# Performance work log

Hardware: AMD Instinct MI355X
Metric: run time of the kernel (lower is better)

Reference implementation:

```python
import jax, jax.numpy as jnp
import numpy as np

B, C, L, D = 32, 1, 1024, 128


def _attention_matrix(x0, x1):
    # x0, x1: [B, 1, L, D]. A[b,0,i,j] = 1 / (1 + ||x0[b,0,i] - x1[b,0,j]||_2)
    a = x0[:, 0]  # [B, L, D]
    b = x1[:, 0]  # [B, L, D]
    # cdist via expansion: ||a_i - b_j||^2 = |a_i|^2 + |b_j|^2 - 2 a_i . b_j
    sq_a = jnp.sum(a * a, axis=-1)                      # [B, L]
    sq_b = jnp.sum(b * b, axis=-1)                      # [B, L]
    inner = jnp.einsum('bid,bjd->bij', a, b)            # [B, L, L]
    d2 = jnp.maximum(sq_a[:, :, None] + sq_b[:, None, :] - 2.0 * inner, 0.0)
    dist = jnp.sqrt(d2)
    A = 1.0 / (1.0 + dist)                              # [B, L, L]
    return A[:, None, :, :]                             # [B, 1, L, L]


def setup_inputs() -> dict:
    key = jax.random.key(0)
    k0, k1, kw0, kw1 = jax.random.split(key, 4)
    x0 = jax.random.normal(k0, (B, C, L, D), dtype=jnp.float32)
    x1 = jax.random.normal(k1, (B, C, L, D), dtype=jnp.float32)
    W0 = jax.random.normal(kw0, (L, D), dtype=jnp.float32)
    W1 = jax.random.normal(kw1, (L, D), dtype=jnp.float32)
    return {"x0": x0, "x1": x1, "W0": W0, "W1": W1}


def reference(x0, x1, W0, W1):
    A = _attention_matrix(x0, x1)                 # [B, 1, L, L]
    A_t = jnp.swapaxes(A, -1, -2)                 # [B, 1, L, L]
    a0 = jnp.matmul(A, W0)                        # [B, 1, L, D]
    a1 = jnp.matmul(A_t, W1)                      # [B, 1, L, D]
    f0 = jnp.concatenate([x0, a0], axis=1)        # [B, 2, L, D]
    f1 = jnp.concatenate([x1, a1], axis=1)        # [B, 2, L, D]
    return (f0, f1)
```

## Files before the change

### kernel.cpp

```cpp
#include <hip/hip_runtime.h>

#define B_ 32
#define L_ 1024
#define D_ 128
#define NT 256

typedef __attribute__((ext_vector_type(8))) short bf8_t;
typedef __attribute__((ext_vector_type(4))) short bf4_t;
typedef __attribute__((ext_vector_type(4))) float f4_t;

__device__ __forceinline__ unsigned cvtpk(float lo, float hi) {
  unsigned r;
  asm("v_cvt_pk_bf16_f32 %0, %1, %2" : "=v"(r) : "v"(lo), "v"(hi));
  return r;
}

__device__ __forceinline__ void gload16(const void* g, void* l) {
  __builtin_amdgcn_global_load_lds((const __attribute__((address_space(1))) void*)g,
                                   (__attribute__((address_space(3))) void*)l, 16, 0, 0);
}

__global__ __launch_bounds__(256)
void prep_kernel(const float* __restrict__ x0, const float* __restrict__ x1,
                 const float* __restrict__ W0, const float* __restrict__ W1,
                 short* __restrict__ Xs, float* __restrict__ sq,
                 short* __restrict__ Wt, float* __restrict__ out) {
  int bid = blockIdx.x;
  if (bid < 8192) {
    int t = bid * 256 + threadIdx.x;
    int row_id = t >> 5;
    int qp = t & 31;
    int which = row_id >> 15;
    int b = (row_id >> 10) & 31;
    int row = row_id & 1023;
    const float* x = which ? x1 : x0;
    float4 v = *(const float4*)(x + ((size_t)b * L_ + row) * D_ + qp * 4);
    float* o = out + (size_t)which * (B_ * 2 * L_ * D_) + (size_t)b * (2 * L_ * D_)
             + (size_t)row * D_ + qp * 4;
    *(float4*)o = v;
    unsigned w0 = cvtpk(v.x, v.y), w1 = cvtpk(v.z, v.w);
    char* xb = (char*)Xs + (size_t)row_id * 256 + ((qp * 8) ^ ((row & 7) << 4));
    *(uint2*)xb = make_uint2(w0, w1);
    float s = v.x * v.x + v.y * v.y + v.z * v.z + v.w * v.w;
    s += __shfl_xor(s, 1); s += __shfl_xor(s, 2); s += __shfl_xor(s, 4);
    s += __shfl_xor(s, 8); s += __shfl_xor(s, 16);
    if (qp == 0) sq[row_id] = s;
  } else {
    int idx = (bid - 8192) * 256 + threadIdx.x;
    int which = idx >> 17;
    int rm = idx & 131071;
    int j32 = rm >> 12;
    int d = (rm >> 5) & 127;
    int jj = rm & 31;
    const float* W = which ? W1 : W0;
    float wv = W[(j32 * 32 + jj) * D_ + d];
    Wt[idx] = (short)(cvtpk(wv, wv) & 0xffffu);
  }
}

__global__ __launch_bounds__(NT, 4)
void fused_attnconv(const short* __restrict__ Xs, const float* __restrict__ sq,
                    const short* __restrict__ Wt, float* __restrict__ out) {
  __shared__ char smem[28672];
  char* Pb = smem + 16384;
  float* sqyL = (float*)(smem + 24576);

  const int bid = blockIdx.x;
  const int x = bid & 7, g = bid >> 3;
  const int p = x + 8 * (g >> 4);
  const int it = g & 15;
  const int which = p >> 5, b = p & 31;
  const int i0 = it * 64;
  const int po = (which ^ 1) * 32 + b;

  const char* apanel = (const char*)Xs + (size_t)p * (L_ * 256);
  const char* ypanel = (const char*)Xs + (size_t)po * (L_ * 256);
  const float* sqx_p = sq + p * L_;
  const float* sqy_p = sq + po * L_;
  float* Oc1 = out + (size_t)which * (B_ * 2 * L_ * D_) + (size_t)b * (2 * L_ * D_) + (L_ * D_);

  const int tid = threadIdx.x;
  const int lane = tid & 63;
  const int w = tid >> 6;
  const int l15 = lane & 15;
  const int q = lane >> 4;
  const int I0 = w * 16;
  const int swz = (l15 & 7) << 4;

  const int yo0 = l15 * 256 + ((0 * 64 + q * 16) ^ swz);
  const int yo1 = l15 * 256 + ((1 * 64 + q * 16) ^ swz);
  const int yo2 = l15 * 256 + ((2 * 64 + q * 16) ^ swz);
  const int yo3 = l15 * 256 + ((3 * 64 + q * 16) ^ swz);
  const int pw0 = (I0 + l15) * 128 + ((q * 8) ^ swz);
  const int pw1 = (I0 + l15) * 128 + ((32 + q * 8) ^ swz);
  const int pro = (I0 + l15) * 128 + ((q * 16) ^ swz);

  bf8_t afr[4];
#pragma unroll
  for (int kb = 0; kb < 4; ++kb)
    afr[kb] = *(const bf8_t*)(apanel + (size_t)(i0 + I0 + l15) * 256 + ((kb * 64 + q * 16) ^ swz));
  const float sxv = sqx_p[i0 + I0 + l15];

  const short* wptr = Wt + which * 131072 + l15 * 32 + q * 8;
  const char* ypref = ypanel + 8192 + (size_t)tid * 16;
  const float* syp = sqyL + q * 4;

  *(f4_t*)(sqyL + tid * 4) = *(const f4_t*)(sqy_p + tid * 4);
  gload16(ypanel + (size_t)tid * 16, smem + tid * 16);
  gload16(ypanel + 4096 + (size_t)tid * 16, smem + 4096 + tid * 16);

  f4_t z4 = {0.f, 0.f, 0.f, 0.f};
  f4_t acc[8];
#pragma unroll
  for (int m = 0; m < 8; ++m) acc[m] = z4;

  __syncthreads();

#pragma unroll 1
  for (int jt = 0; jt < 32; ++jt) {
    char* yB = smem + (jt & 1) * 8192;

    bf8_t wf[8];
#pragma unroll
    for (int m = 0; m < 8; ++m)
      wf[m] = *(const bf8_t*)(wptr + m * 512);
    wptr += 4096;

    if (jt < 31) {
      char* yN = smem + ((jt + 1) & 1) * 8192;
      gload16(ypref, yN + tid * 16);
      gload16(ypref + 4096, yN + 4096 + tid * 16);
    }
    ypref += 8192;

    f4_t sy0 = *(const f4_t*)(syp);
    f4_t sy1 = *(const f4_t*)(syp + 16);
    syp += 32;

    f4_t ST0 = z4, ST1 = z4;
    {
      bf8_t ya = *(const bf8_t*)(yB + yo0);
      bf8_t yb = *(const bf8_t*)(yB + 4096 + yo0);
      ST0 = __builtin_amdgcn_mfma_f32_16x16x32_bf16(ya, afr[0], ST0, 0, 0, 0);
      ST1 = __builtin_amdgcn_mfma_f32_16x16x32_bf16(yb, afr[0], ST1, 0, 0, 0);
      ya = *(const bf8_t*)(yB + yo1);
      yb = *(const bf8_t*)(yB + 4096 + yo1);
      ST0 = __builtin_amdgcn_mfma_f32_16x16x32_bf16(ya, afr[1], ST0, 0, 0, 0);
      ST1 = __builtin_amdgcn_mfma_f32_16x16x32_bf16(yb, afr[1], ST1, 0, 0, 0);
      ya = *(const bf8_t*)(yB + yo2);
      yb = *(const bf8_t*)(yB + 4096 + yo2);
      ST0 = __builtin_amdgcn_mfma_f32_16x16x32_bf16(ya, afr[2], ST0, 0, 0, 0);
      ST1 = __builtin_amdgcn_mfma_f32_16x16x32_bf16(yb, afr[2], ST1, 0, 0, 0);
      ya = *(const bf8_t*)(yB + yo3);
      yb = *(const bf8_t*)(yB + 4096 + yo3);
      ST0 = __builtin_amdgcn_mfma_f32_16x16x32_bf16(ya, afr[3], ST0, 0, 0, 0);
      ST1 = __builtin_amdgcn_mfma_f32_16x16x32_bf16(yb, afr[3], ST1, 0, 0, 0);
    }

    {
      float A0 = __builtin_amdgcn_rcpf(1.0f + __builtin_amdgcn_sqrtf(fmaxf(__builtin_fmaf(-2.f, ST0[0], sxv + sy0[0]), 0.f)));
      float A1 = __builtin_amdgcn_rcpf(1.0f + __builtin_amdgcn_sqrtf(fmaxf(__builtin_fmaf(-2.f, ST0[1], sxv + sy0[1]), 0.f)));
      float A2 = __builtin_amdgcn_rcpf(1.0f + __builtin_amdgcn_sqrtf(fmaxf(__builtin_fmaf(-2.f, ST0[2], sxv + sy0[2]), 0.f)));
      float A3 = __builtin_amdgcn_rcpf(1.0f + __builtin_amdgcn_sqrtf(fmaxf(__builtin_fmaf(-2.f, ST0[3], sxv + sy0[3]), 0.f)));
      union { uint2 u; bf4_t s; } p0;
      p0.u = make_uint2(cvtpk(A0, A1), cvtpk(A2, A3));
      *(bf4_t*)(Pb + pw0) = p0.s;
      float B0 = __builtin_amdgcn_rcpf(1.0f + __builtin_amdgcn_sqrtf(fmaxf(__builtin_fmaf(-2.f, ST1[0], sxv + sy1[0]), 0.f)));
      float B1 = __builtin_amdgcn_rcpf(1.0f + __builtin_amdgcn_sqrtf(fmaxf(__builtin_fmaf(-2.f, ST1[1], sxv + sy1[1]), 0.f)));
      float B2 = __builtin_amdgcn_rcpf(1.0f + __builtin_amdgcn_sqrtf(fmaxf(__builtin_fmaf(-2.f, ST1[2], sxv + sy1[2]), 0.f)));
      float B3 = __builtin_amdgcn_rcpf(1.0f + __builtin_amdgcn_sqrtf(fmaxf(__builtin_fmaf(-2.f, ST1[3], sxv + sy1[3]), 0.f)));
      union { uint2 u; bf4_t s; } p1;
      p1.u = make_uint2(cvtpk(B0, B1), cvtpk(B2, B3));
      *(bf4_t*)(Pb + pw1) = p1.s;
    }

    asm volatile("" ::: "memory");
    __builtin_amdgcn_sched_barrier(0);

    {
      bf8_t pf = *(const bf8_t*)(Pb + pro);
#pragma unroll
      for (int m = 0; m < 8; ++m)
        acc[m] = __builtin_amdgcn_mfma_f32_16x16x32_bf16(pf, wf[m], acc[m], 0, 0, 0);
    }

    __syncthreads();
  }

#pragma unroll
  for (int m = 0; m < 8; ++m) {
    const int d = m * 16 + l15;
#pragma unroll
    for (int r = 0; r < 4; ++r)
      Oc1[(size_t)(i0 + I0 + q * 4 + r) * D_ + d] = acc[m][r];
  }
}

extern "C" void kernel_launch(void* const* d_in, const int* in_sizes, int n_in,
                              void* d_out, int out_size, void* d_ws, size_t ws_size,
                              hipStream_t stream) {
  const float* x0 = (const float*)d_in[0];
  const float* x1 = (const float*)d_in[1];
  const float* W0 = (const float*)d_in[2];
  const float* W1 = (const float*)d_in[3];
  float* out = (float*)d_out;

  char* ws = (char*)d_ws;
  short* Wt = (short*)ws;
  short* Xs = (short*)(ws + 524288);
  float* sq = (float*)(ws + 524288 + 16777216);

  prep_kernel<<<9216, 256, 0, stream>>>(x0, x1, W0, W1, Xs, sq, Wt, out);
  fused_attnconv<<<1024, NT, 0, stream>>>(Xs, sq, Wt, out);
}
```

Measured before the change: 90.46 us.

## Read Y tiles directly from global memory instead of LDS double buffer

```diff
diff --git a/kernel.cpp b/kernel.cpp
--- a/kernel.cpp
+++ b/kernel.cpp
@@ -13,11 +13,6 @@
   unsigned r;
   asm("v_cvt_pk_bf16_f32 %0, %1, %2" : "=v"(r) : "v"(lo), "v"(hi));
   return r;
-}
-
-__device__ __forceinline__ void gload16(const void* g, void* l) {
-  __builtin_amdgcn_global_load_lds((const __attribute__((address_space(1))) void*)g,
-                                   (__attribute__((address_space(3))) void*)l, 16, 0, 0);
 }
 
 __global__ __launch_bounds__(256)
@@ -61,9 +56,7 @@
 __global__ __launch_bounds__(NT, 4)
 void fused_attnconv(const short* __restrict__ Xs, const float* __restrict__ sq,
                     const short* __restrict__ Wt, float* __restrict__ out) {
-  __shared__ char smem[28672];
-  char* Pb = smem + 16384;
-  float* sqyL = (float*)(smem + 24576);
+  __shared__ char Pb[8192];
 
   const int bid = blockIdx.x;
   const int x = bid & 7, g = bid >> 3;
@@ -102,36 +95,21 @@
   const float sxv = sqx_p[i0 + I0 + l15];
 
   const short* wptr = Wt + which * 131072 + l15 * 32 + q * 8;
-  const char* ypref = ypanel + 8192 + (size_t)tid * 16;
-  const float* syp = sqyL + q * 4;
-
-  *(f4_t*)(sqyL + tid * 4) = *(const f4_t*)(sqy_p + tid * 4);
-  gload16(ypanel + (size_t)tid * 16, smem + tid * 16);
-  gload16(ypanel + 4096 + (size_t)tid * 16, smem + 4096 + tid * 16);
+  const char* ytile = ypanel;
+  const float* syp = sqy_p + q * 4;
 
   f4_t z4 = {0.f, 0.f, 0.f, 0.f};
   f4_t acc[8];
 #pragma unroll
   for (int m = 0; m < 8; ++m) acc[m] = z4;
 
-  __syncthreads();
-
 #pragma unroll 1
   for (int jt = 0; jt < 32; ++jt) {
-    char* yB = smem + (jt & 1) * 8192;
-
     bf8_t wf[8];
 #pragma unroll
     for (int m = 0; m < 8; ++m)
       wf[m] = *(const bf8_t*)(wptr + m * 512);
     wptr += 4096;
-
-    if (jt < 31) {
-      char* yN = smem + ((jt + 1) & 1) * 8192;
-      gload16(ypref, yN + tid * 16);
-      gload16(ypref + 4096, yN + 4096 + tid * 16);
-    }
-    ypref += 8192;
 
     f4_t sy0 = *(const f4_t*)(syp);
     f4_t sy1 = *(const f4_t*)(syp + 16);
@@ -139,23 +117,24 @@
 
     f4_t ST0 = z4, ST1 = z4;
     {
-      bf8_t ya = *(const bf8_t*)(yB + yo0);
-      bf8_t yb = *(const bf8_t*)(yB + 4096 + yo0);
+      bf8_t ya = *(const bf8_t*)(ytile + yo0);
+      bf8_t yb = *(const bf8_t*)(ytile + 4096 + yo0);
       ST0 = __builtin_amdgcn_mfma_f32_16x16x32_bf16(ya, afr[0], ST0, 0, 0, 0);
       ST1 = __builtin_amdgcn_mfma_f32_16x16x32_bf16(yb, afr[0], ST1, 0, 0, 0);
-      ya = *(const bf8_t*)(yB + yo1);
-      yb = *(const bf8_t*)(yB + 4096 + yo1);
+      ya = *(const bf8_t*)(ytile + yo1);
+      yb = *(const bf8_t*)(ytile + 4096 + yo1);
       ST0 = __builtin_amdgcn_mfma_f32_16x16x32_bf16(ya, afr[1], ST0, 0, 0, 0);
       ST1 = __builtin_amdgcn_mfma_f32_16x16x32_bf16(yb, afr[1], ST1, 0, 0, 0);
-      ya = *(const bf8_t*)(yB + yo2);
-      yb = *(const bf8_t*)(yB + 4096 + yo2);
+      ya = *(const bf8_t*)(ytile + yo2);
+      yb = *(const bf8_t*)(ytile + 4096 + yo2);
       ST0 = __builtin_amdgcn_mfma_f32_16x16x32_bf16(ya, afr[2], ST0, 0, 0, 0);
       ST1 = __builtin_amdgcn_mfma_f32_16x16x32_bf16(yb, afr[2], ST1, 0, 0, 0);
-      ya = *(const bf8_t*)(yB + yo3);
-      yb = *(const bf8_t*)(yB + 4096 + yo3);
+      ya = *(const bf8_t*)(ytile + yo3);
+      yb = *(const bf8_t*)(ytile + 4096 + yo3);
       ST0 = __builtin_amdgcn_mfma_f32_16x16x32_bf16(ya, afr[3], ST0, 0, 0, 0);
       ST1 = __builtin_amdgcn_mfma_f32_16x16x32_bf16(yb, afr[3], ST1, 0, 0, 0);
     }
+    ytile += 8192;
 
     {
       float A0 = __builtin_amdgcn_rcpf(1.0f + __builtin_amdgcn_sqrtf(fmaxf(__builtin_fmaf(-2.f, ST0[0], sxv + sy0[0]), 0.f)));
@@ -183,8 +162,6 @@
       for (int m = 0; m < 8; ++m)
         acc[m] = __builtin_amdgcn_mfma_f32_16x16x32_bf16(pf, wf[m], acc[m], 0, 0, 0);
     }
-
-    __syncthreads();
   }
 
 #pragma unroll
```

New measurement: 126.4 us. 39.7% more time.
